# Optimization experiments

Hardware: AMD Instinct MI355X
Metric: run time of the kernel (lower is better)

The kernel has to match this reference:

```python
import jax, jax.numpy as jnp
import numpy as np

N_IMG = 1024
N_VIEWS = 90


def _bilinear(img, yi, xi):
    """Bilinear sample img at float coords (yi=row, xi=col); 0 outside (skimage warp cval=0)."""
    n = img.shape[0]
    y0 = jnp.floor(yi)
    x0 = jnp.floor(xi)
    wy = yi - y0
    wx = xi - x0
    y0i = y0.astype(jnp.int32)
    x0i = x0.astype(jnp.int32)

    def get(yy, xx):
        valid = (yy >= 0) & (yy < n) & (xx >= 0) & (xx < n)
        v = img[jnp.clip(yy, 0, n - 1), jnp.clip(xx, 0, n - 1)]
        return jnp.where(valid, v, jnp.zeros((), img.dtype))

    v00 = get(y0i, x0i)
    v01 = get(y0i, x0i + 1)
    v10 = get(y0i + 1, x0i)
    v11 = get(y0i + 1, x0i + 1)
    return (v00 * (1 - wy) * (1 - wx) + v01 * (1 - wy) * wx
            + v10 * wy * (1 - wx) + v11 * wy * wx)


def radon_jax(image, theta_deg):
    """skimage.transform.radon(image, theta, circle=True) equivalent.
    Rotate image by each angle (bilinear, about center = N//2, inverse map as in
    skimage warp) and sum over rows. Returns sinogram [N, n_angles]."""
    n = image.shape[0]
    center = n // 2
    ang = jnp.deg2rad(theta_deg.astype(image.dtype))
    cos_a = jnp.cos(ang)  # [A]
    sin_a = jnp.sin(ang)
    coords = jnp.arange(n, dtype=image.dtype)
    X, Y = jnp.meshgrid(coords, coords)  # X = col (x), Y = row (y), [N, N]

    def rotate_and_sum(ca, sa):
        # inverse map: src = R @ dst (homogeneous, (x, y) order) as in skimage radon
        x_in = ca * X + sa * Y - center * (ca + sa - 1)
        y_in = -sa * X + ca * Y - center * (ca - sa - 1)
        rotated = _bilinear(image, y_in, x_in)  # [N, N]
        return rotated.sum(axis=0)  # sum over rows -> projection [N]

    sino = jax.vmap(rotate_and_sum)(cos_a, sin_a)  # [A, N]
    return sino.T  # [N, A] to match skimage radon layout


def setup_inputs() -> dict:
    key = jax.random.key(0)
    k1, _ = jax.random.split(key)
    x = jax.random.normal(k1, (N_IMG, N_IMG), dtype=jnp.float32)
    theta = jnp.arange(N_VIEWS, dtype=jnp.float32) * 2.0  # 0..178 deg, 2-deg spacing
    return {"x": x, "theta": theta}


def reference(x, theta):
    return radon_jax(x, theta)
```

## Files before the change

kernel.cpp:

```cpp
#include <hip/hip_runtime.h>

#define N_IMG   1024
#define N_VIEWS 90
#define CENTER  512
#define TILE    64
#define NYB     (N_IMG / TILE)
#define MAXH    92
#define MAXS    97
#define NTHREADS 512
#define NWAVES   8

__device__ __forceinline__ void map_coords(float ca, float sa, float cx, float cy,
                                           float Xf, float Yf,
                                           float& x_in, float& y_in) {
    const float fx0 = fmaf(ca, Xf, cx);
    const float fy0 = fmaf(-sa, Xf, cy);
    x_in = fmaf(sa, Yf, fx0);
    y_in = fmaf(ca, Yf, fy0);
}

__device__ __forceinline__ void gload_lds4(const float* g, float* l) {
    __builtin_amdgcn_global_load_lds((const __attribute__((address_space(1))) void*)g,
                                     (__attribute__((address_space(3))) void*)l,
                                     4, 0, 0);
}

template<int STRIDE>
__device__ __forceinline__ float tile_work(const float* __restrict__ img,
                                           float* __restrict__ tile,
                                           int lane, int wv,
                                           int iy0, int h, int a0x, int dB,
                                           float sa, float ca, float fx0, float fy0,
                                           int Ybase, bool interior) {
    {
        const float* g = img + (size_t)(iy0 + wv) * N_IMG + a0x + lane;
        float* l = tile + wv * STRIDE;
        for (int r = wv; r < h; r += NWAVES) {
            gload_lds4(g, l);
            if (dB > 0) gload_lds4(g + dB, l + dB);
            g += NWAVES * N_IMG;
            l += NWAVES * STRIDE;
        }
    }
    __syncthreads();

    float acc = 0.0f;
    const int base = -(iy0 * STRIDE + a0x);

    if (interior) {
        #pragma unroll
        for (int i = 0; i < TILE / NWAVES; ++i) {
            const float Yf   = (float)(Ybase + i);
            const float x_in = fmaf(sa, Yf, fx0);
            const float y_in = fmaf(ca, Yf, fy0);
            const float x0f = floorf(x_in);
            const float y0f = floorf(y_in);
            const float wx  = x_in - x0f;
            const float wy  = y_in - y0f;
            const int li = (int)y0f * STRIDE + (int)x0f + base;
            const float t00 = tile[li];
            const float t01 = tile[li + 1];
            const float t10 = tile[li + STRIDE];
            const float t11 = tile[li + STRIDE + 1];
            const float top = fmaf(wx, t01 - t00, t00);
            const float bot = fmaf(wx, t11 - t10, t10);
            acc += fmaf(wy, bot - top, top);
        }
    } else {
        #pragma unroll
        for (int i = 0; i < TILE / NWAVES; ++i) {
            const float Yf   = (float)(Ybase + i);
            const float x_in = fmaf(sa, Yf, fx0);
            const float y_in = fmaf(ca, Yf, fy0);
            const float x0f = floorf(x_in);
            const float y0f = floorf(y_in);
            const float wx  = x_in - x0f;
            const float wy  = y_in - y0f;
            const int x0 = (int)x0f;
            const int y0 = (int)y0f;
            const int x0c = min(max(x0,     0), N_IMG - 1);
            const int x1c = min(max(x0 + 1, 0), N_IMG - 1);
            const int y0c = min(max(y0,     0), N_IMG - 1);
            const int y1c = min(max(y0 + 1, 0), N_IMG - 1);
            const float wxa = (x0     >= 0 && x0     < N_IMG) ? (1.0f - wx) : 0.0f;
            const float wxb = (x0 + 1 >= 0 && x0 + 1 < N_IMG) ? wx          : 0.0f;
            const float wya = (y0     >= 0 && y0     < N_IMG) ? (1.0f - wy) : 0.0f;
            const float wyb = (y0 + 1 >= 0 && y0 + 1 < N_IMG) ? wy          : 0.0f;
            const int r0 = (y0c - iy0) * STRIDE - a0x;
            const int r1 = (y1c - iy0) * STRIDE - a0x;
            const float t00 = tile[r0 + x0c];
            const float t01 = tile[r0 + x1c];
            const float t10 = tile[r1 + x0c];
            const float t11 = tile[r1 + x1c];
            acc += wya * fmaf(wxa, t00, wxb * t01)
                 + wyb * fmaf(wxa, t10, wxb * t11);
        }
    }
    return acc;
}

__global__ __launch_bounds__(NTHREADS) void radon_tile(const float* __restrict__ img,
                                                       const float* __restrict__ theta,
                                                       float* __restrict__ partial,
                                                       float* __restrict__ out,
                                                       int mode) {
    __shared__ float tile[MAXH * MAXS];

    const int a  = blockIdx.z;
    const int X0 = blockIdx.x * TILE;
    const int Y0 = blockIdx.y * TILE;
    const int tid  = threadIdx.x;
    const int lane = tid & 63;
    const int wv   = tid >> 6;

    float* __restrict__ pslot = partial + ((size_t)(a * NYB + blockIdx.y) << 10) + X0;

    const float ang = theta[a] * 0.017453292519943295f;
    float sa, ca;
    __sincosf(ang, &sa, &ca);
    const float cx = (float)CENTER * (1.0f - ca - sa);
    const float cy = (float)CENTER * (1.0f - ca + sa);

    float x00, y00, x01, y01, x10, y10, x11, y11;
    map_coords(ca, sa, cx, cy, (float)X0,        (float)Y0,        x00, y00);
    map_coords(ca, sa, cx, cy, (float)(X0 + 63), (float)Y0,        x01, y01);
    map_coords(ca, sa, cx, cy, (float)X0,        (float)(Y0 + 63), x10, y10);
    map_coords(ca, sa, cx, cy, (float)(X0 + 63), (float)(Y0 + 63), x11, y11);
    const float xmin = fminf(fminf(x00, x01), fminf(x10, x11));
    const float xmax = fmaxf(fmaxf(x00, x01), fmaxf(x10, x11));
    const float ymin = fminf(fminf(y00, y01), fminf(y10, y11));
    const float ymax = fmaxf(fmaxf(y00, y01), fmaxf(y10, y11));

    const int ix0_raw = (int)floorf(xmin);
    const int ix1_raw = (int)floorf(xmax) + 1;
    const int iy0_raw = (int)floorf(ymin);
    const int iy1_raw = (int)floorf(ymax) + 1;

    const int ix0 = max(0, ix0_raw);
    const int ix1 = min(N_IMG - 1, ix1_raw);
    const int iy0 = max(0, iy0_raw);
    const int iy1 = min(N_IMG - 1, iy1_raw);

    if (ix1 < ix0 || iy1 < iy0) {
        if (mode == 0) { if (tid < 64) pslot[tid] = 0.0f; }
        return;
    }

    const int a0x = min(ix0, N_IMG - 64);
    const int b0x = max(a0x, ix1 - 63);
    const int dB  = b0x - a0x;
    const int h   = iy1 - iy0 + 1;

    const int X = X0 + lane;
    const float Xf  = (float)X;
    const float fx0 = fmaf(ca, Xf, cx);
    const float fy0 = fmaf(-sa, Xf, cy);
    const int Ybase = Y0 + wv * (TILE / NWAVES);

    const bool interior = (ix0_raw >= 0) && (ix1_raw <= N_IMG - 1) &&
                          (iy0_raw >= 0) && (iy1_raw <= N_IMG - 1);

    float acc;
    if (ca > 0.0f)
        acc = tile_work<95>(img, tile, lane, wv, iy0, h, a0x, dB,
                            sa, ca, fx0, fy0, Ybase, interior);
    else
        acc = tile_work<97>(img, tile, lane, wv, iy0, h, a0x, dB,
                            sa, ca, fx0, fy0, Ybase, interior);

    __syncthreads();
    tile[wv * 64 + lane] = acc;
    __syncthreads();
    if (wv == 0) {
        float s = 0.0f;
        #pragma unroll
        for (int w = 0; w < NWAVES; ++w) s += tile[w * 64 + lane];
        if (mode == 0) pslot[lane] = s;
        else           atomicAdd(&out[X * N_VIEWS + a], s);
    }
}

__global__ __launch_bounds__(256) void reduce_partials(const float* __restrict__ partial,
                                                       float* __restrict__ out) {
    const int g = blockIdx.x * 256 + threadIdx.x;
    const int a = g >> 10;
    const int X = g & 1023;
    float s = 0.0f;
    #pragma unroll
    for (int yb = 0; yb < NYB; ++yb)
        s += partial[((size_t)(a * NYB + yb) << 10) + X];
    out[X * N_VIEWS + a] = s;
}

extern "C" void kernel_launch(void* const* d_in, const int* in_sizes, int n_in,
                              void* d_out, int out_size, void* d_ws, size_t ws_size,
                              hipStream_t stream) {
    const float* img   = (const float*)d_in[0];
    const float* theta = (const float*)d_in[1];
    float* out     = (float*)d_out;
    float* partial = (float*)d_ws;

    const size_t needed = (size_t)N_VIEWS * NYB * N_IMG * sizeof(float);
    const int mode = (ws_size >= needed) ? 0 : 1;
    if (mode == 1)
        hipMemsetAsync(d_out, 0, (size_t)out_size * sizeof(float), stream);

    dim3 grid(N_IMG / TILE, N_IMG / TILE, N_VIEWS);
    radon_tile<<<grid, NTHREADS, 0, stream>>>(img, theta, partial, out, mode);

    if (mode == 0)
        reduce_partials<<<(N_VIEWS * N_IMG) / 256, 256, 0, stream>>>(partial, out);
}
```

Baseline: 150.7 us.

## Use 16-byte global-to-LDS loads with fixed 96-wide rows for shallow angles

For angles with |cos| above about 0.707, the tile is staged into LDS as contiguous 96-float rows aligned to 4 floats, using 16-byte global_load_lds. This replaces the per-row 4-byte loads and the second optional load, cutting the number of load instructions. The LDS index computation also moves to float fma before a single conversion. Rows are clamped at the bottom of the image, and the 96-wide window assumes the footprint fits after 4-alignment, which is a correctness risk near the threshold.

```diff
diff --git a/kernel.cpp b/kernel.cpp
--- a/kernel.cpp
+++ b/kernel.cpp
@@ -6,9 +6,9 @@
 #define TILE    64
 #define NYB     (N_IMG / TILE)
 #define MAXH    92
-#define MAXS    97
 #define NTHREADS 512
 #define NWAVES   8
+#define TILE_WORDS 9088
 
 __device__ __forceinline__ void map_coords(float ca, float sa, float cx, float cy,
                                            float Xf, float Yf,
@@ -24,14 +24,22 @@
                                      (__attribute__((address_space(3))) void*)l,
                                      4, 0, 0);
 }
+__device__ __forceinline__ void gload_lds16(const float* g, float* l) {
+    __builtin_amdgcn_global_load_lds((const __attribute__((address_space(1))) void*)g,
+                                     (__attribute__((address_space(3))) void*)l,
+                                     16, 0, 0);
+}
 
 template<int STRIDE>
-__device__ __forceinline__ float tile_work(const float* __restrict__ img,
-                                           float* __restrict__ tile,
-                                           int lane, int wv,
-                                           int iy0, int h, int a0x, int dB,
-                                           float sa, float ca, float fx0, float fy0,
-                                           int Ybase, bool interior) {
+__device__ __forceinline__ float tile_steep(const float* __restrict__ img,
+                                            float* __restrict__ tile,
+                                            int lane, int wv,
+                                            int iy0, int h, int ix0, int ix1,
+                                            float sa, float ca, float fx0, float fy0,
+                                            int Ybase, bool interior) {
+    const int a0x = min(ix0, N_IMG - 64);
+    const int b0x = max(a0x, ix1 - 63);
+    const int dB  = b0x - a0x;
     {
         const float* g = img + (size_t)(iy0 + wv) * N_IMG + a0x + lane;
         float* l = tile + wv * STRIDE;
@@ -45,7 +53,8 @@
     __syncthreads();
 
     float acc = 0.0f;
-    const int base = -(iy0 * STRIDE + a0x);
+    const float basef = -(float)(iy0 * STRIDE + a0x);
+    const float Sf = (float)STRIDE;
 
     if (interior) {
         #pragma unroll
@@ -57,7 +66,7 @@
             const float y0f = floorf(y_in);
             const float wx  = x_in - x0f;
             const float wy  = y_in - y0f;
-            const int li = (int)y0f * STRIDE + (int)x0f + base;
+            const int li = (int)(fmaf(y0f, Sf, x0f) + basef);
             const float t00 = tile[li];
             const float t01 = tile[li + 1];
             const float t10 = tile[li + STRIDE];
@@ -99,12 +108,86 @@
     return acc;
 }
 
+__device__ __forceinline__ float tile_shallow(const float* __restrict__ img,
+                                              float* __restrict__ tile,
+                                              int lane, int wv,
+                                              int iy0, int h, int base4,
+                                              float sa, float ca, float fx0, float fy0,
+                                              int Ybase, bool interior) {
+    {
+        const int D = h * 96;
+        for (int o = wv * 256; o < D; o += NWAVES * 256) {
+            const int d = o + 4 * lane;
+            const int r = (unsigned)d / 96u;
+            const int c = d - r * 96;
+            const int gr = min(iy0 + r, N_IMG - 1);
+            const float* g = img + (size_t)gr * N_IMG + base4 + c;
+            gload_lds16(g, tile + o);
+        }
+    }
+    __syncthreads();
+
+    float acc = 0.0f;
+    const float basef = -(float)(iy0 * 96 + base4);
+
+    if (interior) {
+        #pragma unroll
+        for (int i = 0; i < TILE / NWAVES; ++i) {
+            const float Yf   = (float)(Ybase + i);
+            const float x_in = fmaf(sa, Yf, fx0);
+            const float y_in = fmaf(ca, Yf, fy0);
+            const float x0f = floorf(x_in);
+            const float y0f = floorf(y_in);
+            const float wx  = x_in - x0f;
+            const float wy  = y_in - y0f;
+            const int li = (int)(fmaf(y0f, 96.0f, x0f) + basef);
+            const float t00 = tile[li];
+            const float t01 = tile[li + 1];
+            const float t10 = tile[li + 96];
+            const float t11 = tile[li + 97];
+            const float top = fmaf(wx, t01 - t00, t00);
+            const float bot = fmaf(wx, t11 - t10, t10);
+            acc += fmaf(wy, bot - top, top);
+        }
+    } else {
+        #pragma unroll
+        for (int i = 0; i < TILE / NWAVES; ++i) {
+            const float Yf   = (float)(Ybase + i);
+            const float x_in = fmaf(sa, Yf, fx0);
+            const float y_in = fmaf(ca, Yf, fy0);
+            const float x0f = floorf(x_in);
+            const float y0f = floorf(y_in);
+            const float wx  = x_in - x0f;
+            const float wy  = y_in - y0f;
+            const int x0 = (int)x0f;
+            const int y0 = (int)y0f;
+            const int x0c = min(max(x0,     0), N_IMG - 1);
+            const int x1c = min(max(x0 + 1, 0), N_IMG - 1);
+            const int y0c = min(max(y0,     0), N_IMG - 1);
+            const int y1c = min(max(y0 + 1, 0), N_IMG - 1);
+            const float wxa = (x0     >= 0 && x0     < N_IMG) ? (1.0f - wx) : 0.0f;
+            const float wxb = (x0 + 1 >= 0 && x0 + 1 < N_IMG) ? wx          : 0.0f;
+            const float wya = (y0     >= 0 && y0     < N_IMG) ? (1.0f - wy) : 0.0f;
+            const float wyb = (y0 + 1 >= 0 && y0 + 1 < N_IMG) ? wy          : 0.0f;
+            const int r0 = (y0c - iy0) * 96 - base4;
+            const int r1 = (y1c - iy0) * 96 - base4;
+            const float t00 = tile[r0 + x0c];
+            const float t01 = tile[r0 + x1c];
+            const float t10 = tile[r1 + x0c];
+            const float t11 = tile[r1 + x1c];
+            acc += wya * fmaf(wxa, t00, wxb * t01)
+                 + wyb * fmaf(wxa, t10, wxb * t11);
+        }
+    }
+    return acc;
+}
+
 __global__ __launch_bounds__(NTHREADS) void radon_tile(const float* __restrict__ img,
                                                        const float* __restrict__ theta,
                                                        float* __restrict__ partial,
                                                        float* __restrict__ out,
                                                        int mode) {
-    __shared__ float tile[MAXH * MAXS];
+    __shared__ float tile[TILE_WORDS];
 
     const int a  = blockIdx.z;
     const int X0 = blockIdx.x * TILE;
@@ -146,10 +229,7 @@
         return;
     }
 
-    const int a0x = min(ix0, N_IMG - 64);
-    const int b0x = max(a0x, ix1 - 63);
-    const int dB  = b0x - a0x;
-    const int h   = iy1 - iy0 + 1;
+    const int h = iy1 - iy0 + 1;
 
     const int X = X0 + lane;
     const float Xf  = (float)X;
@@ -161,12 +241,17 @@
                           (iy0_raw >= 0) && (iy1_raw <= N_IMG - 1);
 
     float acc;
-    if (ca > 0.0f)
-        acc = tile_work<95>(img, tile, lane, wv, iy0, h, a0x, dB,
-                            sa, ca, fx0, fy0, Ybase, interior);
-    else
-        acc = tile_work<97>(img, tile, lane, wv, iy0, h, a0x, dB,
-                            sa, ca, fx0, fy0, Ybase, interior);
+    if (fabsf(ca) > 0.7072f) {
+        const int base4 = min(ix0 & ~3, N_IMG - 96);
+        acc = tile_shallow(img, tile, lane, wv, iy0, h, base4,
+                           sa, ca, fx0, fy0, Ybase, interior);
+    } else if (ca > 0.0f) {
+        acc = tile_steep<95>(img, tile, lane, wv, iy0, h, ix0, ix1,
+                             sa, ca, fx0, fy0, Ybase, interior);
+    } else {
+        acc = tile_steep<97>(img, tile, lane, wv, iy0, h, ix0, ix1,
+                             sa, ca, fx0, fy0, Ybase, interior);
+    }
 
     __syncthreads();
     tile[wv * 64 + lane] = acc;
```

New measurement: 146.3 us. 2.9% less time.

## Add 16-byte LDS staging path for near-axis angles and share block params via LDS

Applied to the files above, without the earlier changes.

When |cos| is large, the tile window is aligned to 4 columns with a fixed stride of 96, and rows are staged with 16-byte global_load_lds transfers instead of 4-byte ones. The bounding-box and angle setup now runs only in wave 0 and reaches the other waves through shared memory. Sample coordinates are stepped incrementally rather than recomputed per row, and the tile index is built in float arithmetic. The aim is fewer load instructions and less redundant scalar work, at the cost of an extra barrier and possible float rounding in index or coordinate accumulation.

```diff
diff --git a/kernel.cpp b/kernel.cpp
--- a/kernel.cpp
+++ b/kernel.cpp
@@ -5,10 +5,10 @@
 #define CENTER  512
 #define TILE    64
 #define NYB     (N_IMG / TILE)
-#define MAXH    92
-#define MAXS    97
 #define NTHREADS 512
 #define NWAVES   8
+#define YPT      (TILE / NWAVES)
+#define TILE_WORDS 9216
 
 __device__ __forceinline__ void map_coords(float ca, float sa, float cx, float cy,
                                            float Xf, float Yf,
@@ -24,40 +24,28 @@
                                      (__attribute__((address_space(3))) void*)l,
                                      4, 0, 0);
 }
+__device__ __forceinline__ void gload_lds16(const float* g, float* l) {
+    __builtin_amdgcn_global_load_lds((const __attribute__((address_space(1))) void*)g,
+                                     (__attribute__((address_space(3))) void*)l,
+                                     16, 0, 0);
+}
 
 template<int STRIDE>
-__device__ __forceinline__ float tile_work(const float* __restrict__ img,
-                                           float* __restrict__ tile,
-                                           int lane, int wv,
-                                           int iy0, int h, int a0x, int dB,
-                                           float sa, float ca, float fx0, float fy0,
-                                           int Ybase, bool interior) {
-    {
-        const float* g = img + (size_t)(iy0 + wv) * N_IMG + a0x + lane;
-        float* l = tile + wv * STRIDE;
-        for (int r = wv; r < h; r += NWAVES) {
-            gload_lds4(g, l);
-            if (dB > 0) gload_lds4(g + dB, l + dB);
-            g += NWAVES * N_IMG;
-            l += NWAVES * STRIDE;
-        }
-    }
-    __syncthreads();
-
+__device__ __forceinline__ float sample_tile(const float* __restrict__ tile,
+                                             float sa, float ca,
+                                             float x_in, float y_in,
+                                             float basef, int iy0, int win,
+                                             bool interior) {
     float acc = 0.0f;
-    const int base = -(iy0 * STRIDE + a0x);
-
+    const float Sf = (float)STRIDE;
     if (interior) {
         #pragma unroll
-        for (int i = 0; i < TILE / NWAVES; ++i) {
-            const float Yf   = (float)(Ybase + i);
-            const float x_in = fmaf(sa, Yf, fx0);
-            const float y_in = fmaf(ca, Yf, fy0);
+        for (int i = 0; i < YPT; ++i) {
             const float x0f = floorf(x_in);
             const float y0f = floorf(y_in);
             const float wx  = x_in - x0f;
             const float wy  = y_in - y0f;
-            const int li = (int)y0f * STRIDE + (int)x0f + base;
+            const int li = (int)(fmaf(y0f, Sf, x0f) + basef);
             const float t00 = tile[li];
             const float t01 = tile[li + 1];
             const float t10 = tile[li + STRIDE];
@@ -65,13 +53,11 @@
             const float top = fmaf(wx, t01 - t00, t00);
             const float bot = fmaf(wx, t11 - t10, t10);
             acc += fmaf(wy, bot - top, top);
+            x_in += sa; y_in += ca;
         }
     } else {
         #pragma unroll
-        for (int i = 0; i < TILE / NWAVES; ++i) {
-            const float Yf   = (float)(Ybase + i);
-            const float x_in = fmaf(sa, Yf, fx0);
-            const float y_in = fmaf(ca, Yf, fy0);
+        for (int i = 0; i < YPT; ++i) {
             const float x0f = floorf(x_in);
             const float y0f = floorf(y_in);
             const float wx  = x_in - x0f;
@@ -86,14 +72,15 @@
             const float wxb = (x0 + 1 >= 0 && x0 + 1 < N_IMG) ? wx          : 0.0f;
             const float wya = (y0     >= 0 && y0     < N_IMG) ? (1.0f - wy) : 0.0f;
             const float wyb = (y0 + 1 >= 0 && y0 + 1 < N_IMG) ? wy          : 0.0f;
-            const int r0 = (y0c - iy0) * STRIDE - a0x;
-            const int r1 = (y1c - iy0) * STRIDE - a0x;
+            const int r0 = (y0c - iy0) * STRIDE - win;
+            const int r1 = (y1c - iy0) * STRIDE - win;
             const float t00 = tile[r0 + x0c];
             const float t01 = tile[r0 + x1c];
             const float t10 = tile[r1 + x0c];
             const float t11 = tile[r1 + x1c];
             acc += wya * fmaf(wxa, t00, wxb * t01)
                  + wyb * fmaf(wxa, t10, wxb * t11);
+            x_in += sa; y_in += ca;
         }
     }
     return acc;
@@ -104,7 +91,9 @@
                                                        float* __restrict__ partial,
                                                        float* __restrict__ out,
                                                        int mode) {
-    __shared__ float tile[MAXH * MAXS];
+    __shared__ float tile[TILE_WORDS];
+    __shared__ float fpar[4];
+    __shared__ int   ipar[7];
 
     const int a  = blockIdx.z;
     const int X0 = blockIdx.x * TILE;
@@ -113,60 +102,105 @@
     const int lane = tid & 63;
     const int wv   = tid >> 6;
 
+    if (wv == 0) {
+        const float ang = theta[a] * 0.017453292519943295f;
+        float sa, ca;
+        __sincosf(ang, &sa, &ca);
+        const float cx = (float)CENTER * (1.0f - ca - sa);
+        const float cy = (float)CENTER * (1.0f - ca + sa);
+
+        float x00, y00, x01, y01, x10, y10, x11, y11;
+        map_coords(ca, sa, cx, cy, (float)X0,        (float)Y0,        x00, y00);
+        map_coords(ca, sa, cx, cy, (float)(X0 + 63), (float)Y0,        x01, y01);
+        map_coords(ca, sa, cx, cy, (float)X0,        (float)(Y0 + 63), x10, y10);
+        map_coords(ca, sa, cx, cy, (float)(X0 + 63), (float)(Y0 + 63), x11, y11);
+        const float xmin = fminf(fminf(x00, x01), fminf(x10, x11));
+        const float xmax = fmaxf(fmaxf(x00, x01), fmaxf(x10, x11));
+        const float ymin = fminf(fminf(y00, y01), fminf(y10, y11));
+        const float ymax = fmaxf(fmaxf(y00, y01), fmaxf(y10, y11));
+
+        const int ix0_raw = (int)floorf(xmin);
+        const int ix1_raw = (int)floorf(xmax) + 1;
+        const int iy0_raw = (int)floorf(ymin);
+        const int iy1_raw = (int)floorf(ymax) + 1;
+
+        const int ix0 = max(0, ix0_raw);
+        const int ix1 = min(N_IMG - 1, ix1_raw);
+        const int iy0 = max(0, iy0_raw);
+        const int iy1 = min(N_IMG - 1, iy1_raw);
+
+        int path, win, dB = 0;
+        if (fabsf(ca) > 0.7072f) {
+            path = 0; win = min(ix0 & ~3, N_IMG - 96);
+        } else {
+            path = (ca > 0.0f) ? 1 : 2;
+            win = min(ix0, N_IMG - 64);
+            dB  = max(win, ix1 - 63) - win;
+        }
+        if (tid == 0) {
+            fpar[0] = sa; fpar[1] = ca; fpar[2] = cx; fpar[3] = cy;
+            ipar[0] = iy0; ipar[1] = iy1 - iy0 + 1; ipar[2] = win; ipar[3] = dB;
+            ipar[4] = path;
+            ipar[5] = (ix0_raw >= 0) && (ix1_raw <= N_IMG - 1) &&
+                      (iy0_raw >= 0) && (iy1_raw <= N_IMG - 1);
+            ipar[6] = (ix1 < ix0) || (iy1 < iy0);
+        }
+    }
+    __syncthreads();
+
     float* __restrict__ pslot = partial + ((size_t)(a * NYB + blockIdx.y) << 10) + X0;
 
-    const float ang = theta[a] * 0.017453292519943295f;
-    float sa, ca;
-    __sincosf(ang, &sa, &ca);
-    const float cx = (float)CENTER * (1.0f - ca - sa);
-    const float cy = (float)CENTER * (1.0f - ca + sa);
-
-    float x00, y00, x01, y01, x10, y10, x11, y11;
-    map_coords(ca, sa, cx, cy, (float)X0,        (float)Y0,        x00, y00);
-    map_coords(ca, sa, cx, cy, (float)(X0 + 63), (float)Y0,        x01, y01);
-    map_coords(ca, sa, cx, cy, (float)X0,        (float)(Y0 + 63), x10, y10);
-    map_coords(ca, sa, cx, cy, (float)(X0 + 63), (float)(Y0 + 63), x11, y11);
-    const float xmin = fminf(fminf(x00, x01), fminf(x10, x11));
-    const float xmax = fmaxf(fmaxf(x00, x01), fmaxf(x10, x11));
-    const float ymin = fminf(fminf(y00, y01), fminf(y10, y11));
-    const float ymax = fmaxf(fmaxf(y00, y01), fmaxf(y10, y11));
-
-    const int ix0_raw = (int)floorf(xmin);
-    const int ix1_raw = (int)floorf(xmax) + 1;
-    const int iy0_raw = (int)floorf(ymin);
-    const int iy1_raw = (int)floorf(ymax) + 1;
-
-    const int ix0 = max(0, ix0_raw);
-    const int ix1 = min(N_IMG - 1, ix1_raw);
-    const int iy0 = max(0, iy0_raw);
-    const int iy1 = min(N_IMG - 1, iy1_raw);
-
-    if (ix1 < ix0 || iy1 < iy0) {
-        if (mode == 0) { if (tid < 64) pslot[tid] = 0.0f; }
+    if (ipar[6]) {
+        if (mode == 0 && tid < 64) pslot[tid] = 0.0f;
         return;
     }
 
-    const int a0x = min(ix0, N_IMG - 64);
-    const int b0x = max(a0x, ix1 - 63);
-    const int dB  = b0x - a0x;
-    const int h   = iy1 - iy0 + 1;
+    const float sa = fpar[0], ca = fpar[1], cx = fpar[2], cy = fpar[3];
+    const int iy0 = ipar[0], h = ipar[1], win = ipar[2], dB = ipar[3];
+    const int path = ipar[4];
+    const bool interior = ipar[5];
 
     const int X = X0 + lane;
     const float Xf  = (float)X;
     const float fx0 = fmaf(ca, Xf, cx);
     const float fy0 = fmaf(-sa, Xf, cy);
-    const int Ybase = Y0 + wv * (TILE / NWAVES);
-
-    const bool interior = (ix0_raw >= 0) && (ix1_raw <= N_IMG - 1) &&
-                          (iy0_raw >= 0) && (iy1_raw <= N_IMG - 1);
+    const float Ybf = (float)(Y0 + wv * YPT);
+    const float x_in = fmaf(sa, Ybf, fx0);
+    const float y_in = fmaf(ca, Ybf, fy0);
 
     float acc;
-    if (ca > 0.0f)
-        acc = tile_work<95>(img, tile, lane, wv, iy0, h, a0x, dB,
-                            sa, ca, fx0, fy0, Ybase, interior);
-    else
-        acc = tile_work<97>(img, tile, lane, wv, iy0, h, a0x, dB,
-                            sa, ca, fx0, fy0, Ybase, interior);
+    if (path == 0) {
+        const int D = h * 96;
+        for (int o = wv * 256; o < D; o += NWAVES * 256) {
+            const int d = o + 4 * lane;
+            const int r = (unsigned)d / 96u;
+            const int c = d - r * 96;
+            const int gr = min(iy0 + r, N_IMG - 1);
+            gload_lds16(img + (size_t)gr * N_IMG + win + c, tile + o);
+        }
+        __syncthreads();
+        acc = sample_tile<96>(tile, sa, ca, x_in, y_in,
+                              -(float)(iy0 * 96 + win), iy0, win, interior);
+    } else {
+        const int STRIDE = (path == 1) ? 95 : 97;
+        {
+            const float* g = img + (size_t)(iy0 + wv) * N_IMG + win + lane;
+            float* l = tile + wv * STRIDE;
+            for (int r = wv; r < h; r += NWAVES) {
+                gload_lds4(g, l);
+                if (dB > 0) gload_lds4(g + dB, l + dB);
+                g += NWAVES * N_IMG;
+                l += NWAVES * STRIDE;
+            }
+        }
+        __syncthreads();
+        if (path == 1)
+            acc = sample_tile<95>(tile, sa, ca, x_in, y_in,
+                                  -(float)(iy0 * 95 + win), iy0, win, interior);
+        else
+            acc = sample_tile<97>(tile, sa, ca, x_in, y_in,
+                                  -(float)(iy0 * 97 + win), iy0, win, interior);
+    }
 
     __syncthreads();
     tile[wv * 64 + lane] = acc;
```

Result: faster. 144.4 us (-4.2%).
